# Kernel optimization log

Measured on AMD Instinct MI355X. Metric: run time of the kernel, lower is better.

## Reference

```python
import jax, jax.numpy as jnp
import numpy as np

N, E, B = 50000, 800000, 64
DIN, H, NH, L = 128, 128, 4, 3
SYM = 64          # symbolic_feature_dim
FD, ED = SYM // 4, H // 4   # feature_dim=16, embed_dim=32
DH = H // NH
EPS = 1e-5

def _ln(x, g, b):
    m = jnp.mean(x, -1, keepdims=True)
    v = jnp.var(x, -1, keepdims=True)
    return (x - m) * jax.lax.rsqrt(v + EPS) * g + b

def setup_inputs() -> dict:
    key = jax.random.key(0)
    ks = jax.random.split(key, 32)
    s = 0.05
    inp = {
        'node_features': jax.random.normal(ks[0], (N, DIN), jnp.float32),
        'symbolic_features': jax.random.normal(ks[1], (B, SYM), jnp.float32),
        'edge_index': jax.random.randint(ks[2], (2, E), 0, N),
        'batch': jnp.sort(jax.random.randint(ks[3], (N,), 0, B)),
        # GraphEncoder params
        'W_in': jax.random.normal(ks[4], (H, DIN)) * s,
        'b_in': jnp.zeros((H,)),
        'sage_Wl': jax.random.normal(ks[5], (L, H, H)) * s,   # lin_l (neighbors, with bias)
        'sage_bl': jnp.zeros((L, H)),
        'sage_Wr': jax.random.normal(ks[6], (L, H, H)) * s,   # lin_r (root, no bias)
        'ln_g': jnp.ones((L, H)), 'ln_b': jnp.zeros((L, H)),
        # AttentionPooling params
        'query': jax.random.normal(ks[7], (H,)),
        'in_proj_W': jax.random.normal(ks[8], (3 * H, H)) * s,
        'in_proj_b': jnp.zeros((3 * H,)),
        'out_W': jax.random.normal(ks[9], (H, H)) * s,
        'out_b': jnp.zeros((H,)),
        # SymbolicFeatureProcessor params (4 stacked encoders)
        'sym_W': jax.random.normal(ks[10], (4, ED, FD)) * s,
        'sym_b': jnp.zeros((4, ED)),
        'symf_W': jax.random.normal(ks[11], (H, H)) * s,
        'symf_b': jnp.zeros((H,)),
        'symf_g': jnp.ones((H,)), 'symf_beta': jnp.zeros((H,)),
        # main fusion
        'fus_W': jax.random.normal(ks[12], (H, 2 * H)) * s,
        'fus_b': jnp.zeros((H,)),
        'fus_g': jnp.ones((H,)), 'fus_beta': jnp.zeros((H,)),
        # 3 output heads stacked (instability, grounding, risk)
        'head_W1': jax.random.normal(ks[13], (3, H // 2, H)) * s,
        'head_b1': jnp.zeros((3, H // 2)),
        'head_W2': jax.random.normal(ks[14], (3, 1, H // 2)) * s,
        'head_b2': jnp.zeros((3, 1)),
    }
    return inp

def reference(node_features, symbolic_features, W_in, b_in, sage_Wl, sage_bl, sage_Wr,
              ln_g, ln_b, query, in_proj_W, in_proj_b, out_W, out_b,
              sym_W, sym_b, symf_W, symf_b, symf_g, symf_beta,
              fus_W, fus_b, fus_g, fus_beta, head_W1, head_b1, head_W2, head_b2,
              edge_index, batch):
    src, dst = edge_index[0], edge_index[1]
    x = jax.nn.relu(node_features @ W_in.T + b_in)                 # [N,H]
    deg = jax.ops.segment_sum(jnp.ones((E, 1), x.dtype), dst, num_segments=N)
    inv_deg = 1.0 / jnp.maximum(deg, 1.0)
    for l in range(L):
        res = x
        agg = jax.ops.segment_sum(x[src], dst, num_segments=N) * inv_deg  # mean aggr
        h = agg @ sage_Wl[l].T + sage_bl[l] + x @ sage_Wr[l].T
        x = jax.nn.relu(_ln(h, ln_g[l], ln_b[l])) + res
    # ---- AttentionPooling: per-graph MHA with a single learned query ----
    Wq, Wk, Wv = jnp.split(in_proj_W, 3, axis=0)
    bq, bk, bv = jnp.split(in_proj_b, 3)
    q = (Wq @ query + bq).reshape(NH, DH)                          # [NH,DH]
    k = (x @ Wk.T + bk).reshape(N, NH, DH)
    v = (x @ Wv.T + bv).reshape(N, NH, DH)
    scores = jnp.einsum('nhd,hd->nh', k, q) / np.sqrt(DH)          # [N,NH]
    smax = jax.ops.segment_max(scores, batch, num_segments=B)      # [B,NH]
    e = jnp.exp(scores - smax[batch])
    den = jax.ops.segment_sum(e, batch, num_segments=B)
    w = e / den[batch]                                              # segment softmax
    pooled = jax.ops.segment_sum(w[:, :, None] * v, batch, num_segments=B)
    g = pooled.reshape(B, H) @ out_W.T + out_b                      # [B,H]
    # ---- SymbolicFeatureProcessor: 4 parallel encoders + fusion ----
    parts = symbolic_features.reshape(B, 4, FD)
    emb = jax.nn.relu(jnp.einsum('bfi,foi->bfo', parts, sym_W) + sym_b)  # [B,4,ED]
    sym = _ln(jax.nn.relu(emb.reshape(B, H) @ symf_W.T + symf_b), symf_g, symf_beta)
    # ---- Fusion + heads ----
    fused = _ln(jax.nn.relu(jnp.concatenate([g, sym], -1) @ fus_W.T + fus_b), fus_g, fus_beta)
    hh = jax.nn.relu(jnp.einsum('bi,koi->kbo', fused, head_W1) + head_b1[:, None, :])
    out = jax.nn.sigmoid(jnp.einsum('kbo,kpo->kbp', hh, head_W2) + head_b2[:, None, :])
    return (out[0], out[1], out[2])
```

## Files before the change

### kernel.cpp

```cpp
#include <hip/hip_runtime.h>


#define H 128
#define PPG 16
#define BKSH 8
#define CH 4096

typedef unsigned short u16;
typedef unsigned char u8;
typedef __attribute__((ext_vector_type(8))) short bf16x8;
typedef __attribute__((ext_vector_type(4))) float f32x4;
typedef __attribute__((ext_vector_type(2))) float f32x2;

__device__ __forceinline__ float b2f(u16 u){ return __uint_as_float(((unsigned)u) << 16); }
__device__ __forceinline__ u16 f2b(float f){
    unsigned x = __float_as_uint(f);
    unsigned r = x + 0x7fffu + ((x >> 16) & 1u);
    return (u16)(r >> 16);
}
__device__ __forceinline__ bf16x8 cvt8(const float* __restrict__ p){
    bf16x8 v;
    #pragma unroll
    for (int j = 0; j < 8; j++) v[j] = (short)f2b(p[j]);
    return v;
}
__device__ __forceinline__ uint2 pk_fp8(const float* nv){
    int lo = 0, hi = 0;
    lo = __builtin_amdgcn_cvt_pk_fp8_f32(nv[0], nv[1], lo, false);
    lo = __builtin_amdgcn_cvt_pk_fp8_f32(nv[2], nv[3], lo, true);
    hi = __builtin_amdgcn_cvt_pk_fp8_f32(nv[4], nv[5], hi, false);
    hi = __builtin_amdgcn_cvt_pk_fp8_f32(nv[6], nv[7], hi, true);
    uint2 r; r.x = (unsigned)lo; r.y = (unsigned)hi; return r;
}
__device__ __forceinline__ void acc_fp8w(float* ag, unsigned x, unsigned y){
    f32x2 d0 = __builtin_amdgcn_cvt_pk_f32_fp8((int)x, false);
    f32x2 d1 = __builtin_amdgcn_cvt_pk_f32_fp8((int)x, true);
    f32x2 d2 = __builtin_amdgcn_cvt_pk_f32_fp8((int)y, false);
    f32x2 d3 = __builtin_amdgcn_cvt_pk_f32_fp8((int)y, true);
    ag[0] += d0[0]; ag[1] += d0[1];
    ag[2] += d1[0]; ag[3] += d1[1];
    ag[4] += d2[0]; ag[5] += d2[1];
    ag[6] += d3[0]; ag[7] += d3[1];
}
__device__ __forceinline__ int fp8_off(int q, int kk){
    return (kk < 2) ? (q * 16 + kk * 8) : (64 + q * 16 + (kk - 2) * 8);
}
__device__ __forceinline__ void lds_fence(){
    asm volatile("s_waitcnt lgkmcnt(0)" ::: "memory");
    __builtin_amdgcn_sched_barrier(0);
}

__global__ __launch_bounds__(256) void k_splitall(const float* __restrict__ W_in, const float* __restrict__ sWl,
                                                  const float* __restrict__ sWr, const float* __restrict__ ipW,
                                                  u16* __restrict__ Win, u16* __restrict__ Wl,
                                                  u16* __restrict__ Wr, u16* __restrict__ Wv){
    const int WSZ = H * H;
    int i = blockIdx.x * 256 + threadIdx.x;
    if (i < WSZ)               Win[i]           = f2b(W_in[i]);
    else if (i < 4 * WSZ)      Wl[i - WSZ]      = f2b(sWl[i - WSZ]);
    else if (i < 7 * WSZ)      Wr[i - 4 * WSZ]  = f2b(sWr[i - 4 * WSZ]);
    else if (i < 8 * WSZ)      Wv[i - 7 * WSZ]  = f2b(ipW[2 * WSZ + (i - 7 * WSZ)]);
}

__global__ __launch_bounds__(1024) void k_bcnt(const int* __restrict__ dst, int* __restrict__ bcnt,
                                               int E, int NBK){
    __shared__ int cnt[256];
    int tid = threadIdx.x;
    if (tid < 256) cnt[tid] = 0;
    __syncthreads();
    int e0 = blockIdx.x * CH;
    int n = min(CH, E - e0);
    for (int j = tid; j < n; j += 1024) atomicAdd(&cnt[dst[e0 + j] >> BKSH], 1);
    __syncthreads();
    if (tid < NBK && cnt[tid]) atomicAdd(&bcnt[tid], cnt[tid]);
}

__global__ __launch_bounds__(256) void k_bscan(const int* __restrict__ bcnt, int* __restrict__ boff,
                                               int* __restrict__ bcur, int* __restrict__ offs, int NBK, int N){
    __shared__ int pre[256];
    int tid = threadIdx.x;
    int v = (tid < NBK) ? bcnt[tid] : 0;
    pre[tid] = v;
    __syncthreads();
    for (int off = 1; off < 256; off <<= 1){
        int a = (tid >= off) ? pre[tid - off] : 0;
        __syncthreads();
        pre[tid] += a;
        __syncthreads();
    }
    int excl = pre[tid] - v;
    if (tid < NBK){ boff[tid] = excl; bcur[tid] = excl; }
    if (tid == 255){
        boff[NBK] = pre[255];
        offs[N] = pre[255];
    }
}

__global__ __launch_bounds__(1024) void k_bscatter(const int* __restrict__ src, const int* __restrict__ dst,
                                                   unsigned* __restrict__ ebuf, int* __restrict__ bcur,
                                                   int E, int NBK){
    __shared__ int cnt[256], pre[256], loc[256], lcur[256], base[256];
    __shared__ unsigned stage[CH];
    int tid = threadIdx.x;
    if (tid < 256){ cnt[tid] = 0; }
    __syncthreads();
    int e0 = blockIdx.x * CH;
    int n = min(CH, E - e0);
    for (int j = tid; j < n; j += 1024) atomicAdd(&cnt[dst[e0 + j] >> BKSH], 1);
    __syncthreads();
    if (tid < NBK) base[tid] = atomicAdd(&bcur[tid], cnt[tid]);
    if (tid < 256) pre[tid] = cnt[tid];
    __syncthreads();
    for (int off = 1; off < 256; off <<= 1){
        int v = (tid < 256 && tid >= off) ? pre[tid - off] : 0;
        __syncthreads();
        if (tid < 256) pre[tid] += v;
        __syncthreads();
    }
    if (tid < 256){ loc[tid] = pre[tid] - cnt[tid]; lcur[tid] = loc[tid]; }
    __syncthreads();
    for (int j = tid; j < n; j += 1024){
        int d = dst[e0 + j], s = src[e0 + j];
        int k = d >> BKSH;
        int p = atomicAdd(&lcur[k], 1);
        stage[p] = (unsigned)d | ((unsigned)s << 16);
    }
    __syncthreads();
    for (int j = tid; j < n; j += 1024){
        unsigned v = stage[j];
        int k = (v & 0xffffu) >> BKSH;
        ebuf[base[k] + (j - loc[k])] = v;
    }
}

__global__ __launch_bounds__(256) void k_bfill(const unsigned* __restrict__ ebuf, const int* __restrict__ boff,
                                               int* __restrict__ offs, int* __restrict__ csr,
                                               float* __restrict__ invdeg, int N){
    __shared__ int deg[256], pre[256], cur[256];
    int k = blockIdx.x, tid = threadIdx.x;
    int node0 = k << BKSH;
    int s0 = boff[k], s1 = boff[k + 1];
    deg[tid] = 0;
    __syncthreads();
    for (int j = s0 + tid; j < s1; j += 256) atomicAdd(&deg[ebuf[j] & 255u], 1);
    __syncthreads();
    pre[tid] = deg[tid];
    __syncthreads();
    for (int off = 1; off < 256; off <<= 1){
        int v = (tid >= off) ? pre[tid - off] : 0;
        __syncthreads();
        pre[tid] += v;
        __syncthreads();
    }
    int excl = pre[tid] - deg[tid];
    int node = node0 + tid;
    if (node < N){
        offs[node] = s0 + excl;
        invdeg[node] = 1.0f / (float)max(deg[tid], 1);
    }
    cur[tid] = s0 + excl;
    __syncthreads();
    for (int j = s0 + tid; j < s1; j += 256){
        unsigned v = ebuf[j];
        int p = atomicAdd(&cur[v & 255u], 1);
        csr[p] = (int)(v >> 16);
    }
}

__global__ void k_start(const int* __restrict__ batch, int* __restrict__ start, int N, int B){
    int n = blockIdx.x * blockDim.x + threadIdx.x;
    if (n >= N) return;
    int b = batch[n];
    int bp = (n == 0) ? -1 : batch[n - 1];
    for (int g = bp + 1; g <= b; g++) start[g] = n;
    if (n == N - 1){ for (int g = b + 1; g <= B; g++) start[g] = N; }
}

__global__ __launch_bounds__(256) void k_gemm0(const float* __restrict__ A, u16* __restrict__ Xb,
                                               u8* __restrict__ X8,
                                               const u16* __restrict__ W1, const float* __restrict__ bias,
                                               int nrows){
    __shared__ float lt[4][16][132];
    const int wave = threadIdx.x >> 6;
    const int l = threadIdx.x & 63;
    const int q = l >> 4;
    const int t = l & 15;
    const int row0 = blockIdx.x * 64 + wave * 16;
    const int rowA = min(row0 + t, nrows - 1);
    bf16x8 a1[4];
    const float* p = A + (size_t)rowA * H + q * 8;
    #pragma unroll
    for (int kk = 0; kk < 4; kk++) a1[kk] = cvt8(p + kk * 32);
    f32x4 acc[8];
    #pragma unroll
    for (int nt = 0; nt < 8; nt++){
        f32x4 c = {0.f, 0.f, 0.f, 0.f};
        const size_t wof = (size_t)(nt * 16 + t) * H + q * 8;
        #pragma unroll
        for (int kk = 0; kk < 4; kk++)
            c = __builtin_amdgcn_mfma_f32_16x16x32_bf16(a1[kk], *(const bf16x8*)(W1 + wof + kk * 32), c, 0, 0, 0);
        acc[nt] = c;
    }
    float bv[8];
    #pragma unroll
    for (int nt = 0; nt < 8; nt++) bv[nt] = bias[nt * 16 + t];
    #pragma unroll
    for (int r = 0; r < 4; r++)
        #pragma unroll
        for (int nt = 0; nt < 8; nt++)
            lt[wave][q * 4 + r][nt * 16 + t] = fmaxf(acc[nt][r] + bv[nt], 0.f);
    lds_fence();
    const int row = row0 + t;
    if (row < nrows){
        #pragma unroll
        for (int kk = 0; kk < 4; kk++){
            const float* lp = &lt[wave][t][q * 8 + kk * 32];
            float4 v0 = *(const float4*)lp;
            float4 v1 = *(const float4*)(lp + 4);
            float nv[8] = {v0.x, v0.y, v0.z, v0.w, v1.x, v1.y, v1.z, v1.w};
            bf16x8 o;
            #pragma unroll
            for (int j = 0; j < 8; j++) o[j] = (short)f2b(nv[j]);
            *(bf16x8*)(Xb + (size_t)row * H + q * 8 + kk * 32) = o;
            *(uint2*)(X8 + (size_t)row * H + fp8_off(q, kk)) = pk_fp8(nv);
        }
    }
}

template<bool FSC>
__global__ __launch_bounds__(64) void k_layer(
    const u16* __restrict__ Xin, const u8* __restrict__ Xin8,
    u16* __restrict__ Xout, u8* __restrict__ Xout8,
    const int* __restrict__ offs, const int* __restrict__ csr, const float* __restrict__ invdeg,
    const u16* __restrict__ W1, const u16* __restrict__ W2,
    const float* __restrict__ bias, const float* __restrict__ lng, const float* __restrict__ lnb,
    u16* __restrict__ Vb, const u16* __restrict__ Wv, const float* __restrict__ vbias,
    const float* __restrict__ qk, const float* __restrict__ qkb, float* __restrict__ scores,
    int nrows)
{
    __shared__ float ltw[16 * 132];
    const int l = threadIdx.x;
    const int q = l >> 4;
    const int t = l & 15;
    const int myrow = blockIdx.x * 16 + t;
    const bool valid = myrow < nrows;
    const int rowA = min(myrow, nrows - 1);

    bf16x8 a2[4];
    {
        const u16* px = Xin + (size_t)rowA * H + q * 8;
        #pragma unroll
        for (int kk = 0; kk < 4; kk++) a2[kk] = *(const bf16x8*)(px + kk * 32);
    }
    float ag[4][8];
    #pragma unroll
    for (int kk = 0; kk < 4; kk++)
        #pragma unroll
        for (int j = 0; j < 8; j++) ag[kk][j] = 0.f;
    int o0 = valid ? offs[myrow] : 0;
    int o1 = valid ? offs[myrow + 1] : 0;
    int i = o0;
    int p0 = 0, p1 = 0, p2 = 0, p3 = 0;
    if (i + 3 < o1){ p0 = csr[i]; p1 = csr[i + 1]; p2 = csr[i + 2]; p3 = csr[i + 3]; }
    while (i + 3 < o1){
        int t0 = p0, t1 = p1, t2 = p2, t3 = p3;
        int nx = i + 4;
        if (nx + 3 < o1){ p0 = csr[nx]; p1 = csr[nx + 1]; p2 = csr[nx + 2]; p3 = csr[nx + 3]; }
        const u8* g0 = Xin8 + (size_t)t0 * H + q * 16;
        const u8* g1 = Xin8 + (size_t)t1 * H + q * 16;
        const u8* g2 = Xin8 + (size_t)t2 * H + q * 16;
        const u8* g3 = Xin8 + (size_t)t3 * H + q * 16;
        uint4 a0 = *(const uint4*)(g0);
        uint4 b0 = *(const uint4*)(g0 + 64);
        uint4 a1v = *(const uint4*)(g1);
        uint4 b1 = *(const uint4*)(g1 + 64);
        uint4 a2v = *(const uint4*)(g2);
        uint4 b2 = *(const uint4*)(g2 + 64);
        uint4 a3 = *(const uint4*)(g3);
        uint4 b3 = *(const uint4*)(g3 + 64);
        acc_fp8w(ag[0], a0.x, a0.y);  acc_fp8w(ag[1], a0.z, a0.w);
        acc_fp8w(ag[2], b0.x, b0.y);  acc_fp8w(ag[3], b0.z, b0.w);
        acc_fp8w(ag[0], a1v.x, a1v.y); acc_fp8w(ag[1], a1v.z, a1v.w);
        acc_fp8w(ag[2], b1.x, b1.y);  acc_fp8w(ag[3], b1.z, b1.w);
        acc_fp8w(ag[0], a2v.x, a2v.y); acc_fp8w(ag[1], a2v.z, a2v.w);
        acc_fp8w(ag[2], b2.x, b2.y);  acc_fp8w(ag[3], b2.z, b2.w);
        acc_fp8w(ag[0], a3.x, a3.y);  acc_fp8w(ag[1], a3.z, a3.w);
        acc_fp8w(ag[2], b3.x, b3.y);  acc_fp8w(ag[3], b3.z, b3.w);
        i = nx;
    }
    for (; i < o1; i++){
        int s = csr[i];
        const u8* gp = Xin8 + (size_t)s * H + q * 16;
        uint4 wa = *(const uint4*)(gp);
        uint4 wb = *(const uint4*)(gp + 64);
        acc_fp8w(ag[0], wa.x, wa.y);  acc_fp8w(ag[1], wa.z, wa.w);
        acc_fp8w(ag[2], wb.x, wb.y);  acc_fp8w(ag[3], wb.z, wb.w);
    }
    float idg = valid ? invdeg[myrow] : 0.f;
    bf16x8 a1[4];
    #pragma unroll
    for (int kk = 0; kk < 4; kk++){
        bf16x8 v;
        #pragma unroll
        for (int j = 0; j < 8; j++) v[j] = (short)f2b(ag[kk][j] * idg);
        a1[kk] = v;
    }

    f32x4 acc[8];
    #pragma unroll
    for (int nt = 0; nt < 8; nt++){
        f32x4 c = {0.f, 0.f, 0.f, 0.f};
        const size_t wof = (size_t)(nt * 16 + t) * H + q * 8;
        #pragma unroll
        for (int kk = 0; kk < 4; kk++)
            c = __builtin_amdgcn_mfma_f32_16x16x32_bf16(a1[kk], *(const bf16x8*)(W1 + wof + kk * 32), c, 0, 0, 0);
        #pragma unroll
        for (int kk = 0; kk < 4; kk++)
            c = __builtin_amdgcn_mfma_f32_16x16x32_bf16(a2[kk], *(const bf16x8*)(W2 + wof + kk * 32), c, 0, 0, 0);
        acc[nt] = c;
    }
    float bv[8], gv[8], lbv[8];
    #pragma unroll
    for (int nt = 0; nt < 8; nt++){
        int col = nt * 16 + t;
        bv[nt] = bias[col]; gv[nt] = lng[col]; lbv[nt] = lnb[col];
    }
    #pragma unroll
    for (int r = 0; r < 4; r++){
        float hv[8], s = 0.f, s2 = 0.f;
        #pragma unroll
        for (int nt = 0; nt < 8; nt++){ float v = acc[nt][r] + bv[nt]; hv[nt] = v; s += v; s2 += v * v; }
        #pragma unroll
        for (int m = 1; m < 16; m <<= 1){ s += __shfl_xor(s, m, 64); s2 += __shfl_xor(s2, m, 64); }
        float mean = s * (1.f / H);
        float var  = s2 * (1.f / H) - mean * mean;
        float rstd = rsqrtf(var + 1e-5f);
        #pragma unroll
        for (int nt = 0; nt < 8; nt++){
            float v = (hv[nt] - mean) * rstd * gv[nt] + lbv[nt];
            ltw[(q * 4 + r) * 132 + nt * 16 + t] = fmaxf(v, 0.f);
        }
    }
    lds_fence();
    bf16x8 xv[4];
    float sc[4] = {0.f, 0.f, 0.f, 0.f};
    #pragma unroll
    for (int kk = 0; kk < 4; kk++){
        const float* lp = ltw + t * 132 + q * 8 + kk * 32;
        float4 v0 = *(const float4*)lp;
        float4 v1 = *(const float4*)(lp + 4);
        float nv[8] = {v0.x, v0.y, v0.z, v0.w, v1.x, v1.y, v1.z, v1.w};
        #pragma unroll
        for (int j = 0; j < 8; j++) nv[j] += b2f((u16)a2[kk][j]);
        bf16x8 o;
        #pragma unroll
        for (int j = 0; j < 8; j++) o[j] = (short)f2b(nv[j]);
        xv[kk] = o;
        if (FSC){
            #pragma unroll
            for (int h = 0; h < 4; h++){
                const float* qp = qk + h * H + q * 8 + kk * 32;
                float4 q0 = *(const float4*)qp;
                float4 q1 = *(const float4*)(qp + 4);
                sc[h] += nv[0] * q0.x + nv[1] * q0.y + nv[2] * q0.z + nv[3] * q0.w
                       + nv[4] * q1.x + nv[5] * q1.y + nv[6] * q1.z + nv[7] * q1.w;
            }
        } else {
            if (valid){
                *(bf16x8*)(Xout + (size_t)myrow * H + q * 8 + kk * 32) = o;
                *(uint2*)(Xout8 + (size_t)myrow * H + fp8_off(q, kk)) = pk_fp8(nv);
            }
        }
    }
    if (FSC){
        #pragma unroll
        for (int h = 0; h < 4; h++){
            sc[h] += __shfl_xor(sc[h], 16, 64);
            sc[h] += __shfl_xor(sc[h], 32, 64);
        }
        if (q == 0 && valid){
            #pragma unroll
            for (int h = 0; h < 4; h++) scores[myrow * 4 + h] = sc[h] + qkb[h];
        }
        f32x4 vacc[8];
        #pragma unroll
        for (int nt = 0; nt < 8; nt++){
            f32x4 c = {0.f, 0.f, 0.f, 0.f};
            const size_t wof = (size_t)(nt * 16 + t) * H + q * 8;
            #pragma unroll
            for (int kk = 0; kk < 4; kk++)
                c = __builtin_amdgcn_mfma_f32_16x16x32_bf16(xv[kk], *(const bf16x8*)(Wv + wof + kk * 32), c, 0, 0, 0);
            vacc[nt] = c;
        }
        float vb2[8];
        #pragma unroll
        for (int nt = 0; nt < 8; nt++) vb2[nt] = vbias[nt * 16 + t];
        #pragma unroll
        for (int r = 0; r < 4; r++)
            #pragma unroll
            for (int nt = 0; nt < 8; nt++)
                ltw[(q * 4 + r) * 132 + nt * 16 + t] = vacc[nt][r] + vb2[nt];
        lds_fence();
        if (valid){
            #pragma unroll
            for (int kk = 0; kk < 4; kk++){
                const float* lp = ltw + t * 132 + q * 8 + kk * 32;
                float4 v0 = *(const float4*)lp;
                float4 v1 = *(const float4*)(lp + 4);
                bf16x8 o;
                o[0] = (short)f2b(v0.x); o[1] = (short)f2b(v0.y);
                o[2] = (short)f2b(v0.z); o[3] = (short)f2b(v0.w);
                o[4] = (short)f2b(v1.x); o[5] = (short)f2b(v1.y);
                o[6] = (short)f2b(v1.z); o[7] = (short)f2b(v1.w);
                *(bf16x8*)(Vb + (size_t)myrow * H + q * 8 + kk * 32) = o;
            }
        }
    }
}

__global__ __launch_bounds__(128) void k_qk(const float* __restrict__ ipW, const float* __restrict__ ipb,
                                            const float* __restrict__ query,
                                            float* __restrict__ qk, float* __restrict__ qkb){
    __shared__ float qs[H];
    int t = threadIdx.x;
    float a = ipb[t];
    for (int c = 0; c < H; c++) a += ipW[t * H + c] * query[c];
    qs[t] = a;
    __syncthreads();
    const float r32 = 0.17677669529663687f;
    #pragma unroll
    for (int h = 0; h < 4; h++){
        float v = 0.f;
        for (int d = 0; d < 32; d++) v += ipW[(H + h * 32 + d) * H + t] * qs[h * 32 + d];
        qk[h * H + t] = v * r32;
    }
    if (t < 4){
        float z = 0.f;
        for (int d = 0; d < 32; d++) z += ipb[H + t * 32 + d] * qs[t * 32 + d];
        qkb[t] = z * r32;
    }
}

__global__ __launch_bounds__(256) void k_smax(const float* __restrict__ scores, const int* __restrict__ start,
                                              float* __restrict__ smax, int B){
    int idx = blockIdx.x * 4 + (threadIdx.x >> 6);
    if (idx >= B * 4) return;
    int b = idx >> 2, h = idx & 3, l = threadIdx.x & 63;
    int s0 = start[b], s1 = start[b + 1];
    float m = -1e30f;
    for (int n = s0 + l; n < s1; n += 64) m = fmaxf(m, scores[n * 4 + h]);
    #pragma unroll
    for (int s = 1; s < 64; s <<= 1) m = fmaxf(m, __shfl_xor(m, s, 64));
    if (l == 0) smax[idx] = m;
}

__global__ __launch_bounds__(128) void k_poolsum(const float* __restrict__ scores, const u16* __restrict__ Vb,
                                                 const int* __restrict__ start, const float* __restrict__ smax,
                                                 float* __restrict__ praw, float* __restrict__ den){
    int b = blockIdx.x / PPG, p = blockIdx.x % PPG;
    int c = threadIdx.x, h = c >> 5;
    int s0 = start[b], s1 = start[b + 1];
    float sm = smax[b * 4 + h];
    float acc = 0.f, se = 0.f;
    for (int n = s0 + p; n < s1; n += PPG){
        float e = expf(scores[n * 4 + h] - sm);
        acc += e * b2f(Vb[(size_t)n * H + c]);
        se += e;
    }
    atomicAdd(&praw[b * H + c], acc);
    if ((c & 31) == 0) atomicAdd(&den[b * 4 + h], se);
}

__global__ __launch_bounds__(128) void k_tail(
    const float* __restrict__ praw, const float* __restrict__ den,
    const float* __restrict__ outW, const float* __restrict__ outb,
    const float* __restrict__ symfeat, const float* __restrict__ symW, const float* __restrict__ symb,
    const float* __restrict__ sfW, const float* __restrict__ sfb, const float* __restrict__ sfg, const float* __restrict__ sfbeta,
    const float* __restrict__ fusW, const float* __restrict__ fusb, const float* __restrict__ fusg, const float* __restrict__ fusbeta,
    const float* __restrict__ hW1, const float* __restrict__ hb1, const float* __restrict__ hW2, const float* __restrict__ hb2,
    float* __restrict__ dout, int B){
    int b = blockIdx.x, t = threadIdx.x;
    __shared__ float P[H], G[H], EMB[H], S[H], F[H], HHs[192], red[H], mm[2];
    float dh = den[b * 4 + (t >> 5)];
    P[t] = (dh > 0.f) ? praw[b * H + t] / dh : 0.f;
    __syncthreads();
    float a = outb[t];
    for (int c = 0; c < H; c++) a += P[c] * outW[t * H + c];
    G[t] = a;
    {
        int f = t >> 5;
        float e = symb[t];
        for (int i = 0; i < 16; i++) e += symfeat[b * 64 + f * 16 + i] * symW[t * 16 + i];
        EMB[t] = fmaxf(e, 0.f);
    }
    __syncthreads();
    float a2 = sfb[t];
    for (int c = 0; c < H; c++) a2 += EMB[c] * sfW[t * H + c];
    a2 = fmaxf(a2, 0.f);
    red[t] = a2; __syncthreads();
    for (int s = 64; s > 0; s >>= 1){ if (t < s) red[t] += red[t + s]; __syncthreads(); }
    if (t == 0) mm[0] = red[0];
    __syncthreads();
    red[t] = a2 * a2; __syncthreads();
    for (int s = 64; s > 0; s >>= 1){ if (t < s) red[t] += red[t + s]; __syncthreads(); }
    if (t == 0) mm[1] = red[0];
    __syncthreads();
    {
        float mean = mm[0] * (1.f / H), var = mm[1] * (1.f / H) - mean * mean;
        float rstd = rsqrtf(var + 1e-5f);
        S[t] = (a2 - mean) * rstd * sfg[t] + sfbeta[t];
    }
    __syncthreads();
    float fu = fusb[t];
    for (int c = 0; c < H; c++) fu += G[c] * fusW[t * 256 + c];
    for (int c = 0; c < H; c++) fu += S[c] * fusW[t * 256 + 128 + c];
    fu = fmaxf(fu, 0.f);
    red[t] = fu; __syncthreads();
    for (int s = 64; s > 0; s >>= 1){ if (t < s) red[t] += red[t + s]; __syncthreads(); }
    if (t == 0) mm[0] = red[0];
    __syncthreads();
    red[t] = fu * fu; __syncthreads();
    for (int s = 64; s > 0; s >>= 1){ if (t < s) red[t] += red[t + s]; __syncthreads(); }
    if (t == 0) mm[1] = red[0];
    __syncthreads();
    {
        float mean = mm[0] * (1.f / H), var = mm[1] * (1.f / H) - mean * mean;
        float rstd = rsqrtf(var + 1e-5f);
        F[t] = (fu - mean) * rstd * fusg[t] + fusbeta[t];
    }
    __syncthreads();
    for (int idx = t; idx < 192; idx += 128){
        float hv = hb1[idx];
        for (int c = 0; c < H; c++) hv += F[c] * hW1[idx * H + c];
        HHs[idx] = fmaxf(hv, 0.f);
    }
    __syncthreads();
    if (t < 3){
        float z = hb2[t];
        for (int o = 0; o < 64; o++) z += HHs[t * 64 + o] * hW2[t * 64 + o];
        dout[t * B + b] = 1.f / (1.f + expf(-z));
    }
}

extern "C" void kernel_launch(void* const* d_in, const int* in_sizes, int n_in,
                              void* d_out, int out_size, void* d_ws, size_t ws_size,
                              hipStream_t stream){
    const float* NF      = (const float*)d_in[0];
    const float* SYMF    = (const float*)d_in[1];
    const int*   EIDX    = (const int*)d_in[2];
    const int*   BATCH   = (const int*)d_in[3];
    const float* W_in    = (const float*)d_in[4];
    const float* b_in    = (const float*)d_in[5];
    const float* sWl     = (const float*)d_in[6];
    const float* sbl     = (const float*)d_in[7];
    const float* sWr     = (const float*)d_in[8];
    const float* lng     = (const float*)d_in[9];
    const float* lnb     = (const float*)d_in[10];
    const float* query   = (const float*)d_in[11];
    const float* ipW     = (const float*)d_in[12];
    const float* ipb     = (const float*)d_in[13];
    const float* outW    = (const float*)d_in[14];
    const float* outb    = (const float*)d_in[15];
    const float* symW    = (const float*)d_in[16];
    const float* symb    = (const float*)d_in[17];
    const float* sfW     = (const float*)d_in[18];
    const float* sfb     = (const float*)d_in[19];
    const float* sfg     = (const float*)d_in[20];
    const float* sfbeta  = (const float*)d_in[21];
    const float* fusW    = (const float*)d_in[22];
    const float* fusb    = (const float*)d_in[23];
    const float* fusg    = (const float*)d_in[24];
    const float* fusbeta = (const float*)d_in[25];
    const float* hW1     = (const float*)d_in[26];
    const float* hb1     = (const float*)d_in[27];
    const float* hW2     = (const float*)d_in[28];
    const float* hb2     = (const float*)d_in[29];

    const int N = in_sizes[0] / H;
    const int E = in_sizes[2] / 2;
    const int B = in_sizes[1] / 64;
    const int* esrc = EIDX;
    const int* edst = EIDX + E;
    const int NBK = (N + 255) >> BKSH;

    char* w = (char*)d_ws;
    auto alloc = [&](size_t bytes) -> char* {
        char* p = w; w += (bytes + 255) & ~(size_t)255; return p;
    };
    u16*   X0      = (u16*)alloc((size_t)N * H * 2);
    u16*   X1      = (u16*)alloc((size_t)N * H * 2);
    u8*    X0q     = (u8*)alloc((size_t)N * H);
    u8*    X1q     = (u8*)alloc((size_t)N * H);
    u16*   Vb      = (u16*)alloc((size_t)N * H * 2);
    float* scores  = (float*)alloc((size_t)N * 4 * 4);
    unsigned* ebuf = (unsigned*)alloc((size_t)E * 4);
    char* zbase    = w;
    int* bcnt      = (int*)alloc((size_t)NBK * 4);
    float* praw    = (float*)alloc((size_t)B * H * 4);
    float* den     = (float*)alloc((size_t)B * 4 * 4);
    size_t zbytes  = (size_t)(w - zbase);
    int* boff      = (int*)alloc((size_t)(NBK + 1) * 4);
    int* bcur      = (int*)alloc((size_t)NBK * 4);
    int* offs      = (int*)alloc((size_t)(N + 1) * 4);
    float* invdeg  = (float*)alloc((size_t)N * 4);
    int* csr       = (int*)alloc((size_t)E * 4);
    int* start     = (int*)alloc((size_t)(B + 1) * 4);
    float* smax    = (float*)alloc((size_t)B * 4 * 4);
    float* qk      = (float*)alloc((size_t)4 * H * 4);
    float* qkb     = (float*)alloc(4 * 4);
    const int WSZ  = H * H;
    u16* Win = (u16*)alloc(WSZ * 2);
    u16* Wl  = (u16*)alloc(3 * WSZ * 2);
    u16* Wr  = (u16*)alloc(3 * WSZ * 2);
    u16* Wv  = (u16*)alloc(WSZ * 2);

    hipMemsetAsync(zbase, 0, zbytes, stream);

    const int cb = (E + CH - 1) / CH;
    k_bcnt<<<cb, 1024, 0, stream>>>(edst, bcnt, E, NBK);
    k_bscan<<<1, 256, 0, stream>>>(bcnt, boff, bcur, offs, NBK, N);
    k_bscatter<<<cb, 1024, 0, stream>>>(esrc, edst, ebuf, bcur, E, NBK);
    k_bfill<<<NBK, 256, 0, stream>>>(ebuf, boff, offs, csr, invdeg, N);
    k_start<<<(N + 255) / 256, 256, 0, stream>>>(BATCH, start, N, B);
    k_qk<<<1, 128, 0, stream>>>(ipW, ipb, query, qk, qkb);
    k_splitall<<<(8 * WSZ + 255) / 256, 256, 0, stream>>>(W_in, sWl, sWr, ipW, Win, Wl, Wr, Wv);

    const int gb = (N + 63) / 64;
    const int lb = (N + 15) / 16;
    k_gemm0<<<gb, 256, 0, stream>>>(NF, X0, X0q, Win, b_in, N);
    k_layer<false><<<lb, 64, 0, stream>>>(X0, X0q, X1, X1q, offs, csr, invdeg,
                                          Wl + 0 * WSZ, Wr + 0 * WSZ,
                                          sbl + 0 * H, lng + 0 * H, lnb + 0 * H,
                                          nullptr, nullptr, nullptr,
                                          nullptr, nullptr, nullptr, N);
    k_layer<false><<<lb, 64, 0, stream>>>(X1, X1q, X0, X0q, offs, csr, invdeg,
                                          Wl + 1 * WSZ, Wr + 1 * WSZ,
                                          sbl + 1 * H, lng + 1 * H, lnb + 1 * H,
                                          nullptr, nullptr, nullptr,
                                          nullptr, nullptr, nullptr, N);
    k_layer<true><<<lb, 64, 0, stream>>>(X0, X0q, nullptr, nullptr, offs, csr, invdeg,
                                         Wl + 2 * WSZ, Wr + 2 * WSZ,
                                         sbl + 2 * H, lng + 2 * H, lnb + 2 * H,
                                         Vb, Wv, ipb + 2 * H,
                                         qk, qkb, scores, N);
    k_smax<<<B, 256, 0, stream>>>(scores, start, smax, B);
    k_poolsum<<<B * PPG, 128, 0, stream>>>(scores, Vb, start, smax, praw, den);
    k_tail<<<B, 128, 0, stream>>>(praw, den, outW, outb, SYMF, symW, symb,
                                  sfW, sfb, sfg, sfbeta, fusW, fusb, fusg, fusbeta,
                                  hW1, hb1, hW2, hb2, (float*)d_out, B);
}
```

Baseline: 398.5 us.

## Split neighbor aggregation across two waves and vectorize pooling loads

Each layer block now runs two waves that each gather half of every row's neighbor list, and the second wave's partial sums are merged through shared memory before wave 0 does the MFMA epilogue. The goal is more memory-level parallelism and occupancy for the latency-bound fp8 gather. In exchange it adds a block barrier, LDS traffic, and an idle second wave during the GEMM phase. Separately, the pooling kernel reads two bf16 values per thread with 64 threads instead of one value with 128, which also doubles its atomic adds per thread.

```diff
diff --git a/kernel.cpp b/kernel.cpp
--- a/kernel.cpp
+++ b/kernel.cpp
@@ -228,7 +228,7 @@
 }
 
 template<bool FSC>
-__global__ __launch_bounds__(64) void k_layer(
+__global__ __launch_bounds__(128) void k_layer(
     const u16* __restrict__ Xin, const u8* __restrict__ Xin8,
     u16* __restrict__ Xout, u8* __restrict__ Xout8,
     const int* __restrict__ offs, const int* __restrict__ csr, const float* __restrict__ invdeg,
@@ -239,7 +239,8 @@
     int nrows)
 {
     __shared__ float ltw[16 * 132];
-    const int l = threadIdx.x;
+    const int wave = threadIdx.x >> 6;
+    const int l = threadIdx.x & 63;
     const int q = l >> 4;
     const int t = l & 15;
     const int myrow = blockIdx.x * 16 + t;
@@ -247,7 +248,7 @@
     const int rowA = min(myrow, nrows - 1);
 
     bf16x8 a2[4];
-    {
+    if (wave == 0){
         const u16* px = Xin + (size_t)rowA * H + q * 8;
         #pragma unroll
         for (int kk = 0; kk < 4; kk++) a2[kk] = *(const bf16x8*)(px + kk * 32);
@@ -259,13 +260,15 @@
         for (int j = 0; j < 8; j++) ag[kk][j] = 0.f;
     int o0 = valid ? offs[myrow] : 0;
     int o1 = valid ? offs[myrow + 1] : 0;
-    int i = o0;
+    int mid = o0 + ((o1 - o0 + 1) >> 1);
+    int i  = wave ? mid : o0;
+    int ie = wave ? o1 : mid;
     int p0 = 0, p1 = 0, p2 = 0, p3 = 0;
-    if (i + 3 < o1){ p0 = csr[i]; p1 = csr[i + 1]; p2 = csr[i + 2]; p3 = csr[i + 3]; }
-    while (i + 3 < o1){
+    if (i + 3 < ie){ p0 = csr[i]; p1 = csr[i + 1]; p2 = csr[i + 2]; p3 = csr[i + 3]; }
+    while (i + 3 < ie){
         int t0 = p0, t1 = p1, t2 = p2, t3 = p3;
         int nx = i + 4;
-        if (nx + 3 < o1){ p0 = csr[nx]; p1 = csr[nx + 1]; p2 = csr[nx + 2]; p3 = csr[nx + 3]; }
+        if (nx + 3 < ie){ p0 = csr[nx]; p1 = csr[nx + 1]; p2 = csr[nx + 2]; p3 = csr[nx + 3]; }
         const u8* g0 = Xin8 + (size_t)t0 * H + q * 16;
         const u8* g1 = Xin8 + (size_t)t1 * H + q * 16;
         const u8* g2 = Xin8 + (size_t)t2 * H + q * 16;
@@ -288,7 +291,7 @@
         acc_fp8w(ag[2], b3.x, b3.y);  acc_fp8w(ag[3], b3.z, b3.w);
         i = nx;
     }
-    for (; i < o1; i++){
+    for (; i < ie; i++){
         int s = csr[i];
         const u8* gp = Xin8 + (size_t)s * H + q * 16;
         uint4 wa = *(const uint4*)(gp);
@@ -296,6 +299,23 @@
         acc_fp8w(ag[0], wa.x, wa.y);  acc_fp8w(ag[1], wa.z, wa.w);
         acc_fp8w(ag[2], wb.x, wb.y);  acc_fp8w(ag[3], wb.z, wb.w);
     }
+    if (wave == 1){
+        float* pw = ltw + t * 132 + q * 8;
+        #pragma unroll
+        for (int kk = 0; kk < 4; kk++)
+            #pragma unroll
+            for (int j = 0; j < 8; j++) pw[kk * 32 + j] = ag[kk][j];
+    }
+    __syncthreads();
+    if (wave == 1) return;
+    {
+        const float* pr = ltw + t * 132 + q * 8;
+        #pragma unroll
+        for (int kk = 0; kk < 4; kk++)
+            #pragma unroll
+            for (int j = 0; j < 8; j++) ag[kk][j] += pr[kk * 32 + j];
+    }
+    lds_fence();
     float idg = valid ? invdeg[myrow] : 0.f;
     bf16x8 a1[4];
     #pragma unroll
@@ -454,21 +474,25 @@
     if (l == 0) smax[idx] = m;
 }
 
-__global__ __launch_bounds__(128) void k_poolsum(const float* __restrict__ scores, const u16* __restrict__ Vb,
-                                                 const int* __restrict__ start, const float* __restrict__ smax,
-                                                 float* __restrict__ praw, float* __restrict__ den){
+__global__ __launch_bounds__(64) void k_poolsum(const float* __restrict__ scores, const u16* __restrict__ Vb,
+                                                const int* __restrict__ start, const float* __restrict__ smax,
+                                                float* __restrict__ praw, float* __restrict__ den){
     int b = blockIdx.x / PPG, p = blockIdx.x % PPG;
-    int c = threadIdx.x, h = c >> 5;
+    int c2 = threadIdx.x;
+    int h = c2 >> 4;
     int s0 = start[b], s1 = start[b + 1];
     float sm = smax[b * 4 + h];
-    float acc = 0.f, se = 0.f;
+    float a0 = 0.f, a1 = 0.f, se = 0.f;
     for (int n = s0 + p; n < s1; n += PPG){
         float e = expf(scores[n * 4 + h] - sm);
-        acc += e * b2f(Vb[(size_t)n * H + c]);
+        unsigned wv = *(const unsigned*)(Vb + (size_t)n * H + 2 * c2);
+        a0 += e * b2f((u16)(wv & 0xffffu));
+        a1 += e * b2f((u16)(wv >> 16));
         se += e;
     }
-    atomicAdd(&praw[b * H + c], acc);
-    if ((c & 31) == 0) atomicAdd(&den[b * 4 + h], se);
+    atomicAdd(&praw[b * H + 2 * c2], a0);
+    atomicAdd(&praw[b * H + 2 * c2 + 1], a1);
+    if ((c2 & 15) == 0) atomicAdd(&den[b * 4 + h], se);
 }
 
 __global__ __launch_bounds__(128) void k_tail(
@@ -628,23 +652,23 @@
     const int gb = (N + 63) / 64;
     const int lb = (N + 15) / 16;
     k_gemm0<<<gb, 256, 0, stream>>>(NF, X0, X0q, Win, b_in, N);
-    k_layer<false><<<lb, 64, 0, stream>>>(X0, X0q, X1, X1q, offs, csr, invdeg,
-                                          Wl + 0 * WSZ, Wr + 0 * WSZ,
-                                          sbl + 0 * H, lng + 0 * H, lnb + 0 * H,
-                                          nullptr, nullptr, nullptr,
-                                          nullptr, nullptr, nullptr, N);
-    k_layer<false><<<lb, 64, 0, stream>>>(X1, X1q, X0, X0q, offs, csr, invdeg,
-                                          Wl + 1 * WSZ, Wr + 1 * WSZ,
-                                          sbl + 1 * H, lng + 1 * H, lnb + 1 * H,
-                                          nullptr, nullptr, nullptr,
-                                          nullptr, nullptr, nullptr, N);
-    k_layer<true><<<lb, 64, 0, stream>>>(X0, X0q, nullptr, nullptr, offs, csr, invdeg,
-                                         Wl + 2 * WSZ, Wr + 2 * WSZ,
-                                         sbl + 2 * H, lng + 2 * H, lnb + 2 * H,
-                                         Vb, Wv, ipb + 2 * H,
-                                         qk, qkb, scores, N);
+    k_layer<false><<<lb, 128, 0, stream>>>(X0, X0q, X1, X1q, offs, csr, invdeg,
+                                           Wl + 0 * WSZ, Wr + 0 * WSZ,
+                                           sbl + 0 * H, lng + 0 * H, lnb + 0 * H,
+                                           nullptr, nullptr, nullptr,
+                                           nullptr, nullptr, nullptr, N);
+    k_layer<false><<<lb, 128, 0, stream>>>(X1, X1q, X0, X0q, offs, csr, invdeg,
+                                           Wl + 1 * WSZ, Wr + 1 * WSZ,
+                                           sbl + 1 * H, lng + 1 * H, lnb + 1 * H,
+                                           nullptr, nullptr, nullptr,
+                                           nullptr, nullptr, nullptr, N);
+    k_layer<true><<<lb, 128, 0, stream>>>(X0, X0q, nullptr, nullptr, offs, csr, invdeg,
+                                          Wl + 2 * WSZ, Wr + 2 * WSZ,
+                                          sbl + 2 * H, lng + 2 * H, lnb + 2 * H,
+                                          Vb, Wv, ipb + 2 * H,
+                                          qk, qkb, scores, N);
     k_smax<<<B, 256, 0, stream>>>(scores, start, smax, B);
-    k_poolsum<<<B * PPG, 128, 0, stream>>>(scores, Vb, start, smax, praw, den);
+    k_poolsum<<<B * PPG, 64, 0, stream>>>(scores, Vb, start, smax, praw, den);
     k_tail<<<B, 128, 0, stream>>>(praw, den, outW, outb, SYMF, symW, symb,
                                   sfW, sfb, sfg, sfbeta, fusW, fusb, fusg, fusbeta,
                                   hW1, hb1, hW2, hb2, (float*)d_out, B);
```

New measurement: 400.3 us. Within noise of the previous version (+0.4%).
